# Kernel tuning notes

Hardware: AMD Instinct MI355X
Metric: run time of the kernel (lower is better)

## Reference

```python
import jax, jax.numpy as jnp
import numpy as np

B, N, H, D, DEPTH = 16, 1024, 2, 128, 3
A = H * D  # atten_dim = 256
FFN = 1024
EPS = 1e-5


def layer_norm(x, g, b):
    mu = jnp.mean(x, axis=-1, keepdims=True)
    var = jnp.mean(jnp.square(x - mu), axis=-1, keepdims=True)
    return (x - mu) * jax.lax.rsqrt(var + EPS) * g + b


def setup_inputs() -> dict:
    key = jax.random.key(0)
    ks = jax.random.split(key, 16)
    s = lambda fan_in: 1.0 / np.sqrt(fan_in)
    inp = {
        "X": jax.random.normal(ks[0], (B, N, A), jnp.float32),
        # per-layer attention projections, stacked over depth
        "Wq": jax.random.normal(ks[1], (DEPTH, A, A), jnp.float32) * s(A),
        "bq": jnp.zeros((DEPTH, A), jnp.float32),
        "Wk": jax.random.normal(ks[2], (DEPTH, A, A), jnp.float32) * s(A),
        "bk": jnp.zeros((DEPTH, A), jnp.float32),
        "Wv": jax.random.normal(ks[3], (DEPTH, A, A), jnp.float32) * s(A),
        "bv": jnp.zeros((DEPTH, A), jnp.float32),
        # per-layer FFN (roll_out): Linear(A,1024)+ReLU, Linear(1024,A)+ReLU
        "W1": jax.random.normal(ks[4], (DEPTH, A, FFN), jnp.float32) * s(A),
        "b1": jnp.zeros((DEPTH, FFN), jnp.float32),
        "W2": jax.random.normal(ks[5], (DEPTH, FFN, A), jnp.float32) * s(FFN),
        "b2": jnp.zeros((DEPTH, A), jnp.float32),
        # single shared LayerNorm (the torch module reuses one instance)
        "ln_g": jnp.ones((A,), jnp.float32),
        "ln_b": jnp.zeros((A,), jnp.float32),
        # Conv1d(A, A, kernel_size=1) == per-position linear over channels
        "Wc": jax.random.normal(ks[6], (A, A), jnp.float32) * s(A),
        "bc": jnp.zeros((A,), jnp.float32),
        # final Linear(A, A) on pooled features
        "We": jax.random.normal(ks[7], (A, A), jnp.float32) * s(A),
        "be": jnp.zeros((A,), jnp.float32),
    }
    return inp


def reference(X, Wq, bq, Wk, bk, Wv, bv, W1, b1, W2, b2, ln_g, ln_b, Wc, bc, We, be):
    inv_sqrt_d = 1.0 / np.sqrt(D)
    step = X  # [B, N, A]
    for i in range(DEPTH):
        q = (step @ Wq[i] + bq[i]).reshape(B, N, H, D).transpose(0, 2, 1, 3)
        k = (step @ Wk[i] + bk[i]).reshape(B, N, H, D).transpose(0, 2, 1, 3)
        v = (step @ Wv[i] + bv[i]).reshape(B, N, H, D).transpose(0, 2, 1, 3)
        scores = jnp.einsum('bhqd,bhkd->bhqk', q, k) * inv_sqrt_d
        probs = jax.nn.softmax(scores, axis=-1)
        attn = jnp.einsum('bhqk,bhkd->bhqd', probs, v)
        attn = attn.transpose(0, 2, 1, 3).reshape(B, N, A)
        roll = jax.nn.relu(jax.nn.relu(attn @ W1[i] + b1[i]) @ W2[i] + b2[i])
        step = layer_norm(roll + step, ln_g, ln_b)
    # Conv1d(kernel=1) + ReLU over channels, per position
    entity_encodings = jax.nn.relu(step @ Wc + bc)  # [B, N, A]
    pooled = jnp.mean(entity_encodings, axis=1)      # [B, A]
    encoded_entities = jax.nn.relu(pooled @ We + be)  # [B, A]
    return encoded_entities
```

## Files before the change

kernel.cpp:

```cpp
#include <hip/hip_runtime.h>
#include <hip/hip_bf16.h>
#include <cstddef>

#define B_   16
#define N_   1024
#define H_   2
#define D_   128
#define A_   256
#define FFN_ 1024
#define M_   (B_ * N_)
#define EPS_ 1e-5f
#define SPLIT 2
#define KT   32
#define TPC  (N_ / SPLIT / KT)
#define QKV_E ((size_t)B_ * H_ * N_ * D_)

typedef short  short8  __attribute__((ext_vector_type(8)));
typedef float  f32x16  __attribute__((ext_vector_type(16)));
typedef unsigned int uint;
typedef unsigned short ushort;

#define MFMA32(a, b, c) __builtin_amdgcn_mfma_f32_32x32x16_bf16(a, b, c, 0, 0, 0)

__device__ __forceinline__ uint f2b1(float x) {
    uint u = __float_as_uint(x);
    return (u + 0x7fffu + ((u >> 16) & 1u)) >> 16;
}
__device__ __forceinline__ uint f2b2(float lo, float hi) {
    return f2b1(lo) | (f2b1(hi) << 16);
}
__device__ __forceinline__ float b2f(ushort u) {
    return __uint_as_float(((uint)u) << 16);
}

__global__ __launch_bounds__(256) void f32_to_bf16_kernel(
    const float* __restrict__ in, ushort* __restrict__ out)
{
    const size_t i = ((size_t)blockIdx.x * 256 + threadIdx.x) * 8;
    float4 a = *(const float4*)(in + i);
    float4 b = *(const float4*)(in + i + 4);
    uint4 w = { f2b2(a.x, a.y), f2b2(a.z, a.w), f2b2(b.x, b.y), f2b2(b.z, b.w) };
    *(uint4*)(out + i) = w;
}

__global__ __launch_bounds__(256) void prep_kernel(
    const float* __restrict__ Wq, const float* __restrict__ Wk,
    const float* __restrict__ Wv, const float* __restrict__ W1,
    const float* __restrict__ W2, const float* __restrict__ Wc,
    ushort* __restrict__ wqkv_t, ushort* __restrict__ w1_t,
    ushort* __restrict__ w2_t, ushort* __restrict__ wc_t)
{
    const int z = blockIdx.z;
    const float* W; ushort* out; int K, N, n0, k0;
    if (z < 9) {
        const int layer = z / 3, sec = z % 3;
        W = (sec == 0 ? Wq : sec == 1 ? Wk : Wv) + (size_t)layer * A_ * A_;
        out = wqkv_t + (size_t)layer * 3 * A_ * A_ + (size_t)sec * A_ * A_;
        K = A_; N = A_;
        n0 = blockIdx.x * 32; k0 = blockIdx.y * 32;
    } else if (z < 12) {
        const int layer = z - 9;
        W = W1 + (size_t)layer * A_ * FFN_; out = w1_t + (size_t)layer * A_ * FFN_;
        K = A_; N = FFN_;
        n0 = blockIdx.x * 32; k0 = blockIdx.y * 32;
    } else if (z < 15) {
        const int layer = z - 12;
        W = W2 + (size_t)layer * FFN_ * A_; out = w2_t + (size_t)layer * FFN_ * A_;
        K = FFN_; N = A_;
        k0 = blockIdx.x * 32; n0 = blockIdx.y * 32;
    } else {
        W = Wc; out = wc_t; K = A_; N = A_;
        n0 = blockIdx.x * 32; k0 = blockIdx.y * 32;
    }
    if (n0 >= N || k0 >= K) return;

    __shared__ float tile[32][33];
    const int tc = threadIdx.x & 31, tr = threadIdx.x >> 5;
#pragma unroll
    for (int it = 0; it < 4; ++it) {
        int r = it * 8 + tr;
        tile[r][tc] = W[(size_t)(k0 + r) * N + n0 + tc];
    }
    __syncthreads();
#pragma unroll
    for (int it = 0; it < 4; ++it) {
        int r = it * 8 + tr;
        out[(size_t)(n0 + r) * K + k0 + tc] = (ushort)f2b1(tile[tc][r]);
    }
}

template <int MR>
__global__ __launch_bounds__(256) void gemm_mfma(
    const ushort* __restrict__ Asrc, const ushort* __restrict__ Wt,
    const float* __restrict__ bias, const float* __restrict__ biasK,
    const float* __restrict__ biasV, void* __restrict__ outp,
    int Kloop, int lda, int ldc, int mode)
{
    constexpr int BM = MR * 64;
    __shared__ ushort sA[BM * 72];
    __shared__ ushort sB[128 * 72];

    const int tid = threadIdx.x;
    const int wid = tid >> 6, lane = tid & 63;
    const int c = lane & 31, g = lane >> 5;
    const int wr = wid >> 1, wc = wid & 1;
    const int m0 = blockIdx.x * BM;
    const int n0 = blockIdx.y * 128;

    size_t zout = 0;
    if (mode == 7) {
        const int h = blockIdx.z;
        Asrc += (size_t)h * Kloop;
        Wt   += (size_t)h * Kloop;
        zout  = (size_t)h * M_ * A_;
    }

    f32x16 acc[MR][2] = {};

    for (int k0 = 0; k0 < Kloop; k0 += 64) {
        __syncthreads();
#pragma unroll
        for (int it = 0; it < BM / 32; ++it) {
            int idx = it * 256 + tid, r = idx >> 3, cc = (idx & 7) * 8;
            *(uint4*)&sA[r * 72 + cc] =
                *(const uint4*)(Asrc + (size_t)(m0 + r) * lda + k0 + cc);
        }
#pragma unroll
        for (int it = 0; it < 4; ++it) {
            int idx = it * 256 + tid, r = idx >> 3, cc = (idx & 7) * 8;
            *(uint4*)&sB[r * 72 + cc] =
                *(const uint4*)(Wt + (size_t)(n0 + r) * lda + k0 + cc);
        }
        __syncthreads();
#pragma unroll
        for (int ks = 0; ks < 4; ++ks) {
            const int ko = ks * 16 + 8 * g;
            short8 b0 = *(const short8*)&sB[(wc * 64 + c) * 72 + ko];
            short8 b1 = *(const short8*)&sB[(wc * 64 + 32 + c) * 72 + ko];
#pragma unroll
            for (int mr = 0; mr < MR; ++mr) {
                short8 a = *(const short8*)&sA[((wr * MR + mr) * 32 + c) * 72 + ko];
                acc[mr][0] = MFMA32(a, b0, acc[mr][0]);
                acc[mr][1] = MFMA32(a, b1, acc[mr][1]);
            }
        }
    }

    const int sec = n0 >> 8;
    const float* bp = bias;
    int nw = n0;
    if (mode == 5) {
        bp = (sec == 0 ? bias : sec == 1 ? biasK : biasV);
        nw = n0 & 255;
    }
    const float bz[2] = { bp[nw + wc * 64 + c], bp[nw + wc * 64 + 32 + c] };

    float colsum[2] = { 0.f, 0.f };

#pragma unroll
    for (int mr = 0; mr < MR; ++mr) {
#pragma unroll
        for (int ct = 0; ct < 2; ++ct) {
            const int colbase = n0 + wc * 64 + ct * 32 + c;
            const float addb = (mode == 7) ? 0.f : bz[ct];
#pragma unroll
            for (int rg = 0; rg < 4; ++rg) {
                const int row = m0 + (wr * MR + mr) * 32 + 8 * rg + 4 * g;
                float v0 = acc[mr][ct][4 * rg + 0] + addb;
                float v1 = acc[mr][ct][4 * rg + 1] + addb;
                float v2 = acc[mr][ct][4 * rg + 2] + addb;
                float v3 = acc[mr][ct][4 * rg + 3] + addb;
                if (mode == 1 || mode == 2 || mode == 6) {
                    v0 = fmaxf(v0, 0.f); v1 = fmaxf(v1, 0.f);
                    v2 = fmaxf(v2, 0.f); v3 = fmaxf(v3, 0.f);
                }
                if (mode == 1) {
                    float* o = (float*)outp;
                    o[(size_t)(row + 0) * ldc + colbase] = v0;
                    o[(size_t)(row + 1) * ldc + colbase] = v1;
                    o[(size_t)(row + 2) * ldc + colbase] = v2;
                    o[(size_t)(row + 3) * ldc + colbase] = v3;
                } else if (mode == 2 || mode == 7) {
                    ushort* o = (ushort*)outp + zout;
                    o[(size_t)(row + 0) * ldc + colbase] = (ushort)f2b1(v0);
                    o[(size_t)(row + 1) * ldc + colbase] = (ushort)f2b1(v1);
                    o[(size_t)(row + 2) * ldc + colbase] = (ushort)f2b1(v2);
                    o[(size_t)(row + 3) * ldc + colbase] = (ushort)f2b1(v3);
                } else if (mode == 6) {
                    colsum[ct] += v0 + v1 + v2 + v3;
                } else {
                    const int cw = colbase & 255;
                    const int hh = cw >> 7, dd = cw & (D_ - 1);
                    if (sec < 2) {
                        ushort* o = (ushort*)outp + (size_t)sec * QKV_E;
#pragma unroll
                        for (int r2 = 0; r2 < 4; ++r2) {
                            int rw = row + r2;
                            int bb = rw >> 10, np = rw & (N_ - 1);
                            float vv = (r2 == 0 ? v0 : r2 == 1 ? v1 : r2 == 2 ? v2 : v3);
                            size_t off = (((size_t)(bb * H_ + hh) * 32 + (np >> 5)) * 16
                                          + (dd >> 3)) * 256
                                         + (np & 31) * 8 + (dd & 7);
                            o[off] = (ushort)f2b1(vv);
                        }
                    } else {
                        ushort* o = (ushort*)outp + 2 * QKV_E;
                        const int bb = row >> 10, np = row & (N_ - 1);
                        size_t off = ((((size_t)(bb * H_ + hh) * 32 + (np >> 5)) * 4
                                       + (dd >> 5)) * 4 + ((np & 31) >> 3)) * 256
                                     + (dd & 31) * 8 + (np & 7);
                        uint2 w = { f2b2(v0, v1), f2b2(v2, v3) };
                        *(uint2*)(o + off) = w;
                    }
                }
            }
        }
    }

    if (mode == 6) {
        float* part = (float*)outp;
        const int b = m0 >> 10;
#pragma unroll
        for (int ct = 0; ct < 2; ++ct) {
            float cs = colsum[ct] + __shfl_xor(colsum[ct], 32, 64);
            if (g == 0)
                atomicAdd(&part[(size_t)b * A_ + n0 + wc * 64 + ct * 32 + c], cs);
        }
    }
}

#define OPITCH 132

__global__ __launch_bounds__(128, 2) void attn_kernel(
    const ushort* __restrict__ qg, const ushort* __restrict__ kg,
    const ushort* __restrict__ vtg, ushort* __restrict__ po,
    float* __restrict__ pm, float* __restrict__ pl)
{
    __shared__ ushort sO[64 * OPITCH];

    const int tid = threadIdx.x;
    const int w = tid >> 6, lane = tid & 63;
    const int c = lane & 31, g = lane >> 5;

    const int flat = blockIdx.x;
    const int xcd  = flat & 7;
    const int ii   = flat >> 3;
    const int pair = xcd * 8 + (ii & 7);
    const int qt   = ii >> 3;
    const int bh   = pair & 31;
    const int z    = pair >> 5;

    const int q0 = qt * 64 + w * 32;
    const float scale2 = 0.08838834764831845f * 1.44269504f;
    const float THR = 11.5f;
    const int lo8 = c * 8;

    short8 qf[8];
    const ushort* qt_ = qg + ((size_t)bh * 32 + (q0 >> 5)) * 4096;
#pragma unroll
    for (int ks = 0; ks < 8; ++ks)
        qf[ks] = *(const short8*)(qt_ + (2 * ks + g) * 256 + lo8);

    f32x16 oacc[4] = {};
    float m = -1e30f, l = 0.f;

    const size_t chunk0 = ((size_t)bh * 32 + z * TPC) * 4096;
    const ushort* kb0 = kg + chunk0 + g * 256 + lo8;
    short8 kf0 = *(const short8*)(kb0 + 0 * 512);
    short8 kf1 = *(const short8*)(kb0 + 1 * 512);
    short8 kf2 = *(const short8*)(kb0 + 2 * 512);
    short8 kf3 = *(const short8*)(kb0 + 3 * 512);
    short8 kf4 = *(const short8*)(kb0 + 4 * 512);
    short8 kf5 = *(const short8*)(kb0 + 5 * 512);
    short8 kf6 = *(const short8*)(kb0 + 6 * 512);
    short8 kf7 = *(const short8*)(kb0 + 7 * 512);

    for (int t = 0; t < TPC; ++t) {
        const size_t tb = chunk0 + (size_t)t * 4096;

        const ushort* vb = vtg + tb + g * 256 + lo8;
        short8 vfA0 = *(const short8*)(vb + 0 * 1024);
        short8 vfA1 = *(const short8*)(vb + 1 * 1024);
        short8 vfA2 = *(const short8*)(vb + 2 * 1024);
        short8 vfA3 = *(const short8*)(vb + 3 * 1024);
        short8 vfB0 = *(const short8*)(vb + 0 * 1024 + 512);
        short8 vfB1 = *(const short8*)(vb + 1 * 1024 + 512);
        short8 vfB2 = *(const short8*)(vb + 2 * 1024 + 512);
        short8 vfB3 = *(const short8*)(vb + 3 * 1024 + 512);
        __builtin_amdgcn_sched_barrier(0);

        f32x16 sacc = {};
        __builtin_amdgcn_s_setprio(1);
        sacc = MFMA32(kf0, qf[0], sacc);
        sacc = MFMA32(kf1, qf[1], sacc);
        sacc = MFMA32(kf2, qf[2], sacc);
        sacc = MFMA32(kf3, qf[3], sacc);
        sacc = MFMA32(kf4, qf[4], sacc);
        sacc = MFMA32(kf5, qf[5], sacc);
        sacc = MFMA32(kf6, qf[6], sacc);
        sacc = MFMA32(kf7, qf[7], sacc);
        __builtin_amdgcn_s_setprio(0);

        if (t + 1 < TPC) {
            const ushort* kb2 = kg + tb + 4096 + g * 256 + lo8;
            kf0 = *(const short8*)(kb2 + 0 * 512);
            kf1 = *(const short8*)(kb2 + 1 * 512);
            kf2 = *(const short8*)(kb2 + 2 * 512);
            kf3 = *(const short8*)(kb2 + 3 * 512);
            kf4 = *(const short8*)(kb2 + 4 * 512);
            kf5 = *(const short8*)(kb2 + 5 * 512);
            kf6 = *(const short8*)(kb2 + 6 * 512);
            kf7 = *(const short8*)(kb2 + 7 * 512);
        }
        __builtin_amdgcn_sched_barrier(0);

        float p[16];
        float tmax = -1e30f;
#pragma unroll
        for (int r = 0; r < 16; ++r) {
            float s = sacc[r] * scale2;
            p[r] = s;
            tmax = fmaxf(tmax, s);
        }
        tmax = fmaxf(tmax, __shfl_xor(tmax, 32, 64));
        if (!__all(tmax - m <= THR)) {
            const float mnew = fmaxf(m, tmax);
            const float corr = exp2f(m - mnew);
#pragma unroll
            for (int dt = 0; dt < 4; ++dt)
#pragma unroll
                for (int r = 0; r < 16; ++r) oacc[dt][r] *= corr;
            l *= corr;
            m = mnew;
        }
        float tsum = 0.f;
#pragma unroll
        for (int r = 0; r < 16; ++r) {
            p[r] = exp2f(p[r] - m);
            tsum += p[r];
        }
        tsum += __shfl_xor(tsum, 32, 64);
        l += tsum;

        uint pk[8];
#pragma unroll
        for (int pp = 0; pp < 8; ++pp)
            pk[pp] = f2b2(p[2 * pp], p[2 * pp + 1]);

        uint v0 = g ? pk[0] : pk[2];
        uint v1 = g ? pk[1] : pk[3];
        uint v2 = g ? pk[4] : pk[6];
        uint v3 = g ? pk[5] : pk[7];
        uint r0 = (uint)__shfl_xor((int)v0, 32, 64);
        uint r1 = (uint)__shfl_xor((int)v1, 32, 64);
        uint r2 = (uint)__shfl_xor((int)v2, 32, 64);
        uint r3 = (uint)__shfl_xor((int)v3, 32, 64);

        __builtin_amdgcn_s_setprio(1);
#pragma unroll
        for (int kb = 0; kb < 2; ++kb) {
            union { uint u[4]; short8 s; } pf;
            if (kb == 0) {
                pf.u[0] = g ? r0 : pk[0];
                pf.u[1] = g ? r1 : pk[1];
                pf.u[2] = g ? pk[2] : r0;
                pf.u[3] = g ? pk[3] : r1;
            } else {
                pf.u[0] = g ? r2 : pk[4];
                pf.u[1] = g ? r3 : pk[5];
                pf.u[2] = g ? pk[6] : r2;
                pf.u[3] = g ? pk[7] : r3;
            }
            oacc[0] = MFMA32(kb ? vfB0 : vfA0, pf.s, oacc[0]);
            oacc[1] = MFMA32(kb ? vfB1 : vfA1, pf.s, oacc[1]);
            oacc[2] = MFMA32(kb ? vfB2 : vfA2, pf.s, oacc[2]);
            oacc[3] = MFMA32(kb ? vfB3 : vfA3, pf.s, oacc[3]);
        }
        __builtin_amdgcn_s_setprio(0);
    }

    if (lane < 32) {
        pm[(size_t)(z * 32 + bh) * N_ + q0 + c] = m;
        pl[(size_t)(z * 32 + bh) * N_ + q0 + c] = l;
    }
    {
        const int qrl = w * 32 + c;
#pragma unroll
        for (int dt = 0; dt < 4; ++dt)
#pragma unroll
            for (int rg = 0; rg < 4; ++rg) {
                int d = dt * 32 + 8 * rg + 4 * g;
                uint2 pv = { f2b2(oacc[dt][4 * rg + 0], oacc[dt][4 * rg + 1]),
                             f2b2(oacc[dt][4 * rg + 2], oacc[dt][4 * rg + 3]) };
                *(uint2*)&sO[qrl * OPITCH + d] = pv;
            }
    }
    __syncthreads();
    {
        const size_t pbase = ((size_t)(z * 32 + bh) * N_ + qt * 64) * D_;
#pragma unroll
        for (int it = 0; it < 16; ++it) {
            int idx = it * 128 + tid;
            int r = idx >> 5, dgr = (idx & 31) * 4;
            uint2 v = *(const uint2*)&sO[r * OPITCH + dgr];
            *(uint2*)(po + pbase + (size_t)r * D_ + dgr) = v;
        }
    }
}

__global__ __launch_bounds__(256) void combine_kernel(
    const ushort* __restrict__ po, const float* __restrict__ pm,
    const float* __restrict__ pl, ushort* __restrict__ out)
{
    const int idx = blockIdx.x * 256 + threadIdx.x;
    const int row = idx >> 4, d0 = (idx & 15) * 8;
    const int R = B_ * H_ * N_;

    float ms[SPLIT];
    float M = -1e30f;
#pragma unroll
    for (int s = 0; s < SPLIT; ++s) {
        ms[s] = pm[(size_t)s * R + row];
        M = fmaxf(M, ms[s]);
    }
    float L = 0.f;
    float acc[8] = {};
#pragma unroll
    for (int s = 0; s < SPLIT; ++s) {
        float wgt = exp2f(ms[s] - M);
        L += pl[(size_t)s * R + row] * wgt;
        uint4 pv = *(const uint4*)(po + ((size_t)s * R + row) * D_ + d0);
        const ushort* pu = (const ushort*)&pv;
#pragma unroll
        for (int j = 0; j < 8; ++j) acc[j] += b2f(pu[j]) * wgt;
    }
    const float inv = 1.f / L;
    uint4 w;
    w.x = f2b2(acc[0] * inv, acc[1] * inv);
    w.y = f2b2(acc[2] * inv, acc[3] * inv);
    w.z = f2b2(acc[4] * inv, acc[5] * inv);
    w.w = f2b2(acc[6] * inv, acc[7] * inv);
    const int bh = row >> 10, n = row & (N_ - 1);
    const int bb = bh >> 1, hh = bh & 1;
    *(uint4*)(out + ((size_t)(bb * N_ + n)) * A_ + hh * D_ + d0) = w;
}

__global__ __launch_bounds__(256) void add_ln_kernel(
    const ushort* __restrict__ roll0, const ushort* __restrict__ roll1,
    const float* __restrict__ b2, ushort* __restrict__ stepb,
    const float* __restrict__ g, const float* __restrict__ bta)
{
    const int row = blockIdx.x * 4 + (threadIdx.x >> 6);
    const int lane = threadIdx.x & 63, c4 = lane * 4;
    const size_t base = (size_t)row * A_ + c4;

    uint2 ra = *(const uint2*)(roll0 + base);
    uint2 rb = *(const uint2*)(roll1 + base);
    uint2 pb = *(const uint2*)(stepb + base);
    float4 bz = *(const float4*)(b2 + c4);

    float r0 = fmaxf(b2f((ushort)(ra.x & 0xffff)) + b2f((ushort)(rb.x & 0xffff)) + bz.x, 0.f);
    float r1 = fmaxf(b2f((ushort)(ra.x >> 16))    + b2f((ushort)(rb.x >> 16))    + bz.y, 0.f);
    float r2 = fmaxf(b2f((ushort)(ra.y & 0xffff)) + b2f((ushort)(rb.y & 0xffff)) + bz.z, 0.f);
    float r3 = fmaxf(b2f((ushort)(ra.y >> 16))    + b2f((ushort)(rb.y >> 16))    + bz.w, 0.f);

    float v0 = r0 + b2f((ushort)(pb.x & 0xffff));
    float v1 = r1 + b2f((ushort)(pb.x >> 16));
    float v2 = r2 + b2f((ushort)(pb.y & 0xffff));
    float v3 = r3 + b2f((ushort)(pb.y >> 16));

    float s  = v0 + v1 + v2 + v3;
    float s2 = v0 * v0 + v1 * v1 + v2 * v2 + v3 * v3;
#pragma unroll
    for (int o = 32; o > 0; o >>= 1) {
        s  += __shfl_xor(s, o, 64);
        s2 += __shfl_xor(s2, o, 64);
    }
    const float mu = s * (1.f / A_);
    const float rs = rsqrtf(s2 * (1.f / A_) - mu * mu + EPS_);

    float4 gv = *(const float4*)(g + c4);
    float4 bv = *(const float4*)(bta + c4);
    float y0 = (v0 - mu) * rs * gv.x + bv.x;
    float y1 = (v1 - mu) * rs * gv.y + bv.y;
    float y2 = (v2 - mu) * rs * gv.z + bv.z;
    float y3 = (v3 - mu) * rs * gv.w + bv.w;

    uint2 yb = { f2b2(y0, y1), f2b2(y2, y3) };
    *(uint2*)(stepb + base) = yb;
}

__global__ __launch_bounds__(256) void final_kernel(
    const float* __restrict__ part, const float* __restrict__ We,
    const float* __restrict__ be, float* __restrict__ out)
{
    __shared__ float sp[A_];
    const int b = blockIdx.x, tid = threadIdx.x;
    sp[tid] = part[(size_t)b * A_ + tid] * (1.0f / N_);
    __syncthreads();
    float acc = be[tid];
    for (int kk = 0; kk < A_; ++kk) acc += sp[kk] * We[(size_t)kk * A_ + tid];
    out[b * A_ + tid] = fmaxf(acc, 0.f);
}

extern "C" void kernel_launch(void* const* d_in, const int* in_sizes, int n_in,
                              void* d_out, int out_size, void* d_ws, size_t ws_size,
                              hipStream_t stream)
{
    const float* X    = (const float*)d_in[0];
    const float* Wq   = (const float*)d_in[1];
    const float* bq   = (const float*)d_in[2];
    const float* Wk   = (const float*)d_in[3];
    const float* bk   = (const float*)d_in[4];
    const float* Wv   = (const float*)d_in[5];
    const float* bv   = (const float*)d_in[6];
    const float* W1   = (const float*)d_in[7];
    const float* b1   = (const float*)d_in[8];
    const float* W2   = (const float*)d_in[9];
    const float* b2   = (const float*)d_in[10];
    const float* ln_g = (const float*)d_in[11];
    const float* ln_b = (const float*)d_in[12];
    const float* Wc   = (const float*)d_in[13];
    const float* bc   = (const float*)d_in[14];
    const float* We   = (const float*)d_in[15];
    const float* be   = (const float*)d_in[16];

    char* base = (char*)d_ws;
    ushort* qb     = (ushort*)base;  base += QKV_E * 2;
                             base += QKV_E * 2;
                             base += QKV_E * 2;
    ushort* hbuf   = (ushort*)base;  base += (size_t)M_ * FFN_ * 2;
    ushort* rollp  = (ushort*)base;  base += (size_t)2 * M_ * A_ * 2;
    ushort* stepb  = (ushort*)base;  base += (size_t)M_ * A_ * 2;
    ushort* wqkv_t = (ushort*)base;  base += (size_t)3 * 3 * A_ * A_ * 2;
    ushort* w1_t   = (ushort*)base;  base += (size_t)3 * A_ * FFN_ * 2;
    ushort* w2_t   = (ushort*)base;  base += (size_t)3 * FFN_ * A_ * 2;
    ushort* wc_t   = (ushort*)base;  base += (size_t)A_ * A_ * 2;
    float*  part   = (float*)base;   base += (size_t)B_ * A_ * 4;
    float*  pm     = (float*)base;   base += (size_t)SPLIT * B_ * H_ * N_ * 4;
    float*  pl     = (float*)base;   base += (size_t)SPLIT * B_ * H_ * N_ * 4;
    ushort* kbuf   = qb + QKV_E;
    ushort* vtbuf  = qb + 2 * QKV_E;
    ushort* po     = hbuf;
    ushort* attnb  = qb;

    prep_kernel<<<dim3(32, 8, 16), 256, 0, stream>>>(
        Wq, Wk, Wv, W1, W2, Wc, wqkv_t, w1_t, w2_t, wc_t);
    f32_to_bf16_kernel<<<(M_ * A_) / (256 * 8), 256, 0, stream>>>(X, stepb);

    for (int i = 0; i < 3; ++i) {
        gemm_mfma<2><<<dim3(M_/128, 6), 256, 0, stream>>>(
            stepb, wqkv_t + (size_t)i * 3 * A_ * A_,
            bq + i * A_, bk + i * A_, bv + i * A_, qb, A_, A_, 0, 5);

        attn_kernel<<<16 * SPLIT * B_ * H_, 128, 0, stream>>>(
            qb, kbuf, vtbuf, po, pm, pl);
        combine_kernel<<<(B_*H_*N_*D_)/(256*8), 256, 0, stream>>>(po, pm, pl, attnb);

        gemm_mfma<2><<<dim3(M_/128, FFN_/128), 256, 0, stream>>>(
            attnb, w1_t + (size_t)i * A_ * FFN_, b1 + i * FFN_, nullptr, nullptr,
            hbuf, A_, A_, FFN_, 2);
        gemm_mfma<1><<<dim3(M_/64, A_/128, 2), 256, 0, stream>>>(
            hbuf, w2_t + (size_t)i * FFN_ * A_, b2 + i * A_, nullptr, nullptr,
            rollp, FFN_/2, FFN_, A_, 7);

        add_ln_kernel<<<M_/4, 256, 0, stream>>>(
            rollp, rollp + (size_t)M_ * A_, b2 + i * A_, stepb, ln_g, ln_b);
    }

    hipMemsetAsync(part, 0, (size_t)B_ * A_ * 4, stream);
    gemm_mfma<1><<<dim3(M_/64, A_/128), 256, 0, stream>>>(
        stepb, wc_t, bc, nullptr, nullptr, part, A_, A_, 0, 6);
    final_kernel<<<B_, 256, 0, stream>>>(part, We, be, (float*)d_out);
}
```

Baseline: 337.0 us.

## Remove split-K attention and combine kernel; normalize and write output directly

Drops the two-way split of the key sequence in attention, so each block walks all 1024 keys and normalizes by 1/l before writing bf16 output directly into the [B,N,A] layout. This removes the combine kernel launch, the partial-output, max and sum writes and reads, and the extra rescale pass. In exchange the grid halves to 512 blocks of 128 threads, which reduces parallelism on a 256-CU GPU and doubles the serial loop length per block. The attention output now gets its own buffer instead of aliasing q.

```diff
diff --git a/kernel.cpp b/kernel.cpp
--- a/kernel.cpp
+++ b/kernel.cpp
@@ -10,9 +10,8 @@
 #define FFN_ 1024
 #define M_   (B_ * N_)
 #define EPS_ 1e-5f
-#define SPLIT 2
 #define KT   32
-#define TPC  (N_ / SPLIT / KT)
+#define TPC  (N_ / KT)
 #define QKV_E ((size_t)B_ * H_ * N_ * D_)
 
 typedef short  short8  __attribute__((ext_vector_type(8)));
@@ -233,8 +232,7 @@
 
 __global__ __launch_bounds__(128, 2) void attn_kernel(
     const ushort* __restrict__ qg, const ushort* __restrict__ kg,
-    const ushort* __restrict__ vtg, ushort* __restrict__ po,
-    float* __restrict__ pm, float* __restrict__ pl)
+    const ushort* __restrict__ vtg, ushort* __restrict__ outb)
 {
     __shared__ ushort sO[64 * OPITCH];
 
@@ -245,10 +243,8 @@
     const int flat = blockIdx.x;
     const int xcd  = flat & 7;
     const int ii   = flat >> 3;
-    const int pair = xcd * 8 + (ii & 7);
-    const int qt   = ii >> 3;
-    const int bh   = pair & 31;
-    const int z    = pair >> 5;
+    const int bh   = xcd * 4 + (ii & 3);
+    const int qt   = ii >> 2;
 
     const int q0 = qt * 64 + w * 32;
     const float scale2 = 0.08838834764831845f * 1.44269504f;
@@ -264,7 +260,7 @@
     f32x16 oacc[4] = {};
     float m = -1e30f, l = 0.f;
 
-    const size_t chunk0 = ((size_t)bh * 32 + z * TPC) * 4096;
+    const size_t chunk0 = (size_t)bh * 32 * 4096;
     const ushort* kb0 = kg + chunk0 + g * 256 + lo8;
     short8 kf0 = *(const short8*)(kb0 + 0 * 512);
     short8 kf1 = *(const short8*)(kb0 + 1 * 512);
@@ -379,70 +375,30 @@
         __builtin_amdgcn_s_setprio(0);
     }
 
-    if (lane < 32) {
-        pm[(size_t)(z * 32 + bh) * N_ + q0 + c] = m;
-        pl[(size_t)(z * 32 + bh) * N_ + q0 + c] = l;
-    }
     {
+        const float inv = 1.f / l;
         const int qrl = w * 32 + c;
 #pragma unroll
         for (int dt = 0; dt < 4; ++dt)
 #pragma unroll
             for (int rg = 0; rg < 4; ++rg) {
                 int d = dt * 32 + 8 * rg + 4 * g;
-                uint2 pv = { f2b2(oacc[dt][4 * rg + 0], oacc[dt][4 * rg + 1]),
-                             f2b2(oacc[dt][4 * rg + 2], oacc[dt][4 * rg + 3]) };
+                uint2 pv = { f2b2(oacc[dt][4 * rg + 0] * inv, oacc[dt][4 * rg + 1] * inv),
+                             f2b2(oacc[dt][4 * rg + 2] * inv, oacc[dt][4 * rg + 3] * inv) };
                 *(uint2*)&sO[qrl * OPITCH + d] = pv;
             }
     }
     __syncthreads();
     {
-        const size_t pbase = ((size_t)(z * 32 + bh) * N_ + qt * 64) * D_;
+        const int bb = bh >> 1, hh = bh & 1;
 #pragma unroll
         for (int it = 0; it < 16; ++it) {
             int idx = it * 128 + tid;
             int r = idx >> 5, dgr = (idx & 31) * 4;
             uint2 v = *(const uint2*)&sO[r * OPITCH + dgr];
-            *(uint2*)(po + pbase + (size_t)r * D_ + dgr) = v;
-        }
-    }
-}
-
-__global__ __launch_bounds__(256) void combine_kernel(
-    const ushort* __restrict__ po, const float* __restrict__ pm,
-    const float* __restrict__ pl, ushort* __restrict__ out)
-{
-    const int idx = blockIdx.x * 256 + threadIdx.x;
-    const int row = idx >> 4, d0 = (idx & 15) * 8;
-    const int R = B_ * H_ * N_;
-
-    float ms[SPLIT];
-    float M = -1e30f;
-#pragma unroll
-    for (int s = 0; s < SPLIT; ++s) {
-        ms[s] = pm[(size_t)s * R + row];
-        M = fmaxf(M, ms[s]);
-    }
-    float L = 0.f;
-    float acc[8] = {};
-#pragma unroll
-    for (int s = 0; s < SPLIT; ++s) {
-        float wgt = exp2f(ms[s] - M);
-        L += pl[(size_t)s * R + row] * wgt;
-        uint4 pv = *(const uint4*)(po + ((size_t)s * R + row) * D_ + d0);
-        const ushort* pu = (const ushort*)&pv;
-#pragma unroll
-        for (int j = 0; j < 8; ++j) acc[j] += b2f(pu[j]) * wgt;
-    }
-    const float inv = 1.f / L;
-    uint4 w;
-    w.x = f2b2(acc[0] * inv, acc[1] * inv);
-    w.y = f2b2(acc[2] * inv, acc[3] * inv);
-    w.z = f2b2(acc[4] * inv, acc[5] * inv);
-    w.w = f2b2(acc[6] * inv, acc[7] * inv);
-    const int bh = row >> 10, n = row & (N_ - 1);
-    const int bb = bh >> 1, hh = bh & 1;
-    *(uint4*)(out + ((size_t)(bb * N_ + n)) * A_ + hh * D_ + d0) = w;
+            *(uint2*)(outb + ((size_t)(bb * N_ + qt * 64 + r)) * A_ + hh * D_ + dgr) = v;
+        }
+    }
 }
 
 __global__ __launch_bounds__(256) void add_ln_kernel(
@@ -529,6 +485,7 @@
     ushort* qb     = (ushort*)base;  base += QKV_E * 2;
                              base += QKV_E * 2;
                              base += QKV_E * 2;
+    ushort* attnb  = (ushort*)base;  base += (size_t)M_ * A_ * 2;
     ushort* hbuf   = (ushort*)base;  base += (size_t)M_ * FFN_ * 2;
     ushort* rollp  = (ushort*)base;  base += (size_t)2 * M_ * A_ * 2;
     ushort* stepb  = (ushort*)base;  base += (size_t)M_ * A_ * 2;
@@ -537,12 +494,8 @@
     ushort* w2_t   = (ushort*)base;  base += (size_t)3 * FFN_ * A_ * 2;
     ushort* wc_t   = (ushort*)base;  base += (size_t)A_ * A_ * 2;
     float*  part   = (float*)base;   base += (size_t)B_ * A_ * 4;
-    float*  pm     = (float*)base;   base += (size_t)SPLIT * B_ * H_ * N_ * 4;
-    float*  pl     = (float*)base;   base += (size_t)SPLIT * B_ * H_ * N_ * 4;
     ushort* kbuf   = qb + QKV_E;
     ushort* vtbuf  = qb + 2 * QKV_E;
-    ushort* po     = hbuf;
-    ushort* attnb  = qb;
 
     prep_kernel<<<dim3(32, 8, 16), 256, 0, stream>>>(
         Wq, Wk, Wv, W1, W2, Wc, wqkv_t, w1_t, w2_t, wc_t);
@@ -553,9 +506,7 @@
             stepb, wqkv_t + (size_t)i * 3 * A_ * A_,
             bq + i * A_, bk + i * A_, bv + i * A_, qb, A_, A_, 0, 5);
 
-        attn_kernel<<<16 * SPLIT * B_ * H_, 128, 0, stream>>>(
-            qb, kbuf, vtbuf, po, pm, pl);
-        combine_kernel<<<(B_*H_*N_*D_)/(256*8), 256, 0, stream>>>(po, pm, pl, attnb);
+        attn_kernel<<<16 * B_ * H_, 128, 0, stream>>>(qb, kbuf, vtbuf, attnb);
 
         gemm_mfma<2><<<dim3(M_/128, FFN_/128), 256, 0, stream>>>(
             attnb, w1_t + (size_t)i * A_ * FFN_, b1 + i * FFN_, nullptr, nullptr,
```

Result: slower. 352.9 us (+4.7%).
